# Kernel optimization log

Measured on AMD Instinct MI355X. Metric: run time of the kernel, lower is better.

The kernel has to match this reference:

```python
import jax, jax.numpy as jnp
import numpy as np
import math

B, L, WIN, D, H, FF, NL, V, M = 16, 2048, 128, 512, 8, 2048, 3, 32000, 32
HD = D // H
EPS = 1e-5
RECON_W = 0.1

def _ln(x, g, b):
    m = x.mean(-1, keepdims=True)
    v = ((x - m) ** 2).mean(-1, keepdims=True)
    return (x - m) * jax.lax.rsqrt(v + EPS) * g + b

def _denoiser(x_t, t, motif, left, right, glob, time_proj_W, time_proj_b, cond_proj_W, cond_proj_b,
              qkv_W, qkv_b, attn_out_W, attn_out_b, ff1_W, ff1_b, ff2_W, ff2_b,
              ln1_g, ln1_b, ln2_g, ln2_b, out_W, out_b):
    half = D // 2
    freqs = jnp.exp(-math.log(10000.0) * jnp.arange(half) / (half - 1))
    a = t[:, None] * freqs[None, :]
    temb = jnp.concatenate([jnp.sin(a), jnp.cos(a)], -1) @ time_proj_W.T + time_proj_b
    x = x_t + temb[:, None, :]
    cond = jnp.concatenate([motif, left, right, glob], -1) @ cond_proj_W.T + cond_proj_b
    x = jnp.concatenate([cond[:, None, :], x], 1)
    S = x.shape[1]
    for i in range(NL):  # post-norm TransformerEncoderLayer, relu, no dropout (eval)
        qkv = x @ qkv_W[i].T + qkv_b[i]
        q, k, v = jnp.split(qkv, 3, axis=-1)
        q = q.reshape(B, S, H, HD); k = k.reshape(B, S, H, HD); v = v.reshape(B, S, H, HD)
        attn = jax.nn.softmax(jnp.einsum('bqhd,bkhd->bhqk', q, k) / math.sqrt(HD), axis=-1)
        ctx = jnp.einsum('bhqk,bkhd->bqhd', attn, v).reshape(B, S, D)
        x = _ln(x + ctx @ attn_out_W[i].T + attn_out_b[i], ln1_g[i], ln1_b[i])
        h = jax.nn.relu(x @ ff1_W[i].T + ff1_b[i]) @ ff2_W[i].T + ff2_b[i]
        x = _ln(x + h, ln2_g[i], ln2_b[i])
    return x[:, 1:, :] @ out_W.T + out_b

def setup_inputs():
    key = jax.random.key(0)
    ks = jax.random.split(key, 20)
    s = 0.02
    inp = {}
    inp['token_ids'] = jax.random.randint(ks[0], (B, L), 0, V)
    inp['motif_ids'] = jax.random.randint(ks[1], (B, M), 0, V)
    inp['motif_len'] = jax.random.randint(ks[2], (B,), 1, M + 1)
    inp['window_start'] = jax.random.randint(ks[3], (B,), 0, L - WIN)
    lens = jax.random.randint(ks[4], (B,), 1, WIN + 1).at[0].set(WIN)
    inp['window_end'] = inp['window_start'] + lens
    inp['t'] = jax.random.uniform(ks[5], (B,))
    inp['x0'] = jax.random.normal(ks[6], (B, WIN, D))
    inp['embed_table'] = jax.random.normal(ks[7], (V, D)) * s
    inp['decode_W'] = jax.random.normal(ks[8], (V, D)) * s
    inp['decode_b'] = jnp.zeros((V,))
    inp['adapter_W'] = jax.random.normal(ks[9], (D, D)) * s
    inp['adapter_b'] = jnp.zeros((D,))
    inp['time_proj_W'] = jax.random.normal(ks[10], (D, D)) * s
    inp['time_proj_b'] = jnp.zeros((D,))
    inp['cond_proj_W'] = jax.random.normal(ks[11], (D, 4 * D)) * s
    inp['cond_proj_b'] = jnp.zeros((D,))
    inp['qkv_W'] = jax.random.normal(ks[12], (NL, 3 * D, D)) * s
    inp['qkv_b'] = jnp.zeros((NL, 3 * D))
    inp['attn_out_W'] = jax.random.normal(ks[13], (NL, D, D)) * s
    inp['attn_out_b'] = jnp.zeros((NL, D))
    inp['ff1_W'] = jax.random.normal(ks[14], (NL, FF, D)) * s
    inp['ff1_b'] = jnp.zeros((NL, FF))
    inp['ff2_W'] = jax.random.normal(ks[15], (NL, D, FF)) * s
    inp['ff2_b'] = jnp.zeros((NL, D))
    inp['ln1_g'] = jnp.ones((NL, D)); inp['ln1_b'] = jnp.zeros((NL, D))
    inp['ln2_g'] = jnp.ones((NL, D)); inp['ln2_b'] = jnp.zeros((NL, D))
    inp['out_W'] = jax.random.normal(ks[16], (D, D)) * s
    inp['out_b'] = jnp.zeros((D,))
    return inp

def _forward(token_ids, motif_ids, motif_len, window_start, window_end, t, x0,
             embed_table, decode_W, decode_b, adapter_W, adapter_b, den):
    hidden = embed_table[token_ids]  # frozen backbone encode: [B, L, D]
    pos = jnp.arange(L)
    def pool(s, e):  # vectorized masked mean over region [s, e)
        m = ((pos[None, :] >= s[:, None]) & (pos[None, :] < e[:, None])).astype(hidden.dtype)
        return jnp.einsum('bl,bld->bd', m, hidden) / jnp.maximum(m.sum(1, keepdims=True), 1.0)
    left = pool(jnp.zeros_like(window_start), window_start)
    right = pool(window_end, jnp.full_like(window_end, L))
    glob = hidden.mean(1)
    memb = embed_table[motif_ids]
    mmask = (jnp.arange(M)[None, :] < motif_len[:, None]).astype(memb.dtype)
    motif = (memb * mmask[..., None]).sum(1) / jnp.maximum(motif_len.astype(memb.dtype), 1.0)[:, None]
    actual = jnp.clip(window_end - window_start, 0, WIN)
    win_mask = jnp.arange(WIN)[None, :] < actual[:, None]
    idx = jnp.clip(window_start[:, None] + jnp.arange(WIN)[None, :], 0, L - 1)
    x1 = jnp.take_along_axis(hidden, idx[:, :, None], axis=1) * win_mask[..., None]
    x_t = (1 - t[:, None, None]) * x0 + t[:, None, None] * x1
    target_v = x1 - x0
    pred_v = _denoiser(x_t, t, motif, left, right, glob, *den)
    valid = win_mask[..., None].astype(x1.dtype)
    vel = (((pred_v - target_v) ** 2) * valid).sum() / (jnp.maximum(valid.sum(), 1.0) * D)
    pred_x1 = x_t + (1 - t[:, None, None]) * pred_v
    logits = (pred_x1 @ adapter_W.T + adapter_b) @ decode_W.T + decode_b
    labels = jnp.where(win_mask, jnp.take_along_axis(token_ids, idx, axis=1), -100)
    lv = labels != -100
    logp = jax.nn.log_softmax(logits, axis=-1)
    picked = jnp.take_along_axis(logp, jnp.maximum(labels, 0)[..., None], axis=-1)[..., 0]
    recon = -(picked * lv).sum() / jnp.maximum(lv.sum(), 1)
    return vel + RECON_W * recon

def reference(token_ids, motif_ids, motif_len, window_start, window_end, t, x0,
              embed_table, decode_W, decode_b, adapter_W, adapter_b,
              time_proj_W, time_proj_b, cond_proj_W, cond_proj_b, qkv_W, qkv_b,
              attn_out_W, attn_out_b, ff1_W, ff1_b, ff2_W, ff2_b,
              ln1_g, ln1_b, ln2_g, ln2_b, out_W, out_b):
    den = (time_proj_W, time_proj_b, cond_proj_W, cond_proj_b, qkv_W, qkv_b,
           attn_out_W, attn_out_b, ff1_W, ff1_b, ff2_W, ff2_b,
           ln1_g, ln1_b, ln2_g, ln2_b, out_W, out_b)
    return _forward(token_ids, motif_ids, motif_len, window_start, window_end, t, x0,
                    embed_table, decode_W, decode_b, adapter_W, adapter_b, den)
```

## Files before the change

kernel.cpp:

```cpp
#include <hip/hip_runtime.h>
#include <hip/hip_bf16.h>
#include <math.h>

typedef __hip_bfloat16 bf16;

constexpr int cB = 16, cL = 2048, cWIN = 128, cD = 512, cH = 8, cFF = 2048;
constexpr int cNL = 3, cV = 32000, cM = 32;
constexpr int cHD = cD / cH;
constexpr int cS = cWIN + 1;
constexpr float cEPS = 1e-5f;
constexpr float cRECON_W = 0.1f;
constexpr int cNVT = cV / 128;

__device__ __forceinline__ float b2f(bf16 x) { return __bfloat162float(x); }

__device__ __forceinline__ float ldx(const void* p, size_t i, int f32) {
    return f32 ? ((const float*)p)[i]
               : __bfloat162float(((const bf16*)p)[i]);
}

__device__ __forceinline__ unsigned int f2bf(float f) {
    union { float f; unsigned int u; } v; v.f = f;
    unsigned int u = v.u + 0x7FFFu + ((v.u >> 16) & 1u);
    return u >> 16;
}

__device__ __forceinline__ void glds16(const unsigned short* g, unsigned short* l) {
    __builtin_amdgcn_global_load_lds(
        (const __attribute__((address_space(1))) void*)g,
        (__attribute__((address_space(3))) void*)l, 16, 0, 0);
}

typedef short bf16x8 __attribute__((ext_vector_type(8)));
typedef float f32x4  __attribute__((ext_vector_type(4)));

__global__ void detect_kernel(const void* __restrict__ x0raw, int* __restrict__ flag)
{
    const unsigned short* h = (const unsigned short*)x0raw;
    int tid = threadIdx.x;
    int cnt = 0;
    for (int j = tid; j < 8192; j += 256) {
        unsigned short u = h[2 * j];
        int e = (u >> 7) & 0xFF;
        if (e >= 134) cnt++;
    }
    __shared__ int red[256];
    red[tid] = cnt; __syncthreads();
    for (int off = 128; off > 0; off >>= 1) {
        if (tid < off) red[tid] += red[tid + off];
        __syncthreads();
    }
    if (tid == 0) *flag = (red[0] > 400) ? 1 : 0;
}

__global__ __launch_bounds__(512) void pools_part_kernel(
    const int* __restrict__ tok, const int* __restrict__ wstart,
    const int* __restrict__ wend, const void* __restrict__ emb,
    float* __restrict__ part, const int* __restrict__ dflag)
{
    const int f32 = *dflag;
    int chunk = blockIdx.x;
    int b = blockIdx.y;
    int d = threadIdx.x;
    int ws_ = wstart[b], we_ = wend[b];
    float sl = 0.f, sr = 0.f, sg = 0.f;
    int l0 = chunk * 256;
    for (int l = l0; l < l0 + 256; ++l) {
        int t = tok[b * cL + l];
        float h = ldx(emb, (size_t)t * cD + d, f32);
        sg += h;
        if (l < ws_) sl += h;
        if (l >= we_) sr += h;
    }
    size_t base = ((size_t)(b * 8 + chunk)) * 3 * cD;
    part[base + d]            = sl;
    part[base + cD + d]       = sr;
    part[base + 2 * cD + d]   = sg;
}

__global__ __launch_bounds__(512) void pools_combine_kernel(
    const float* __restrict__ part, const int* __restrict__ mids,
    const int* __restrict__ mlen, const int* __restrict__ wstart,
    const int* __restrict__ wend, const void* __restrict__ emb,
    unsigned short* __restrict__ featb, const int* __restrict__ dflag)
{
    const int f32 = *dflag;
    int b = blockIdx.x;
    int d = threadIdx.x;
    int ws_ = wstart[b], we_ = wend[b];
    float sl = 0.f, sr = 0.f, sg = 0.f;
    for (int c = 0; c < 8; ++c) {
        size_t base = ((size_t)(b * 8 + c)) * 3 * cD;
        sl += part[base + d];
        sr += part[base + cD + d];
        sg += part[base + 2 * cD + d];
    }
    int ml = mlen[b];
    float sm = 0.f;
    for (int j = 0; j < cM; ++j) {
        if (j < ml) sm += ldx(emb, (size_t)mids[b * cM + j] * cD + d, f32);
    }
    unsigned short* fr = featb + (size_t)b * (4 * cD);
    fr[d]            = (unsigned short)f2bf(sm / fmaxf((float)ml, 1.f));
    fr[cD + d]       = (unsigned short)f2bf(sl / fmaxf((float)ws_, 1.f));
    fr[2 * cD + d]   = (unsigned short)f2bf(sr / fmaxf((float)(cL - we_), 1.f));
    fr[3 * cD + d]   = (unsigned short)f2bf(sg / (float)cL);
}

__global__ __launch_bounds__(512) void tf_kernel(
    const void* __restrict__ t_arr, unsigned short* __restrict__ tfbb,
    const int* __restrict__ dflag)
{
    const int f32 = *dflag;
    int b = blockIdx.x;
    int j = threadIdx.x;
    float t = ldx(t_arr, b, f32);
    const int half = cD / 2;
    float v;
    if (j < half) {
        float fr = expf(-logf(10000.f) * (float)j / (float)(half - 1));
        v = sinf(t * fr);
    } else {
        float fr = expf(-logf(10000.f) * (float)(j - half) / (float)(half - 1));
        v = cosf(t * fr);
    }
    tfbb[(size_t)b * cD + j] = (unsigned short)f2bf(v);
}

__global__ __launch_bounds__(512) void build_x_kernel(
    const int* __restrict__ tok, const int* __restrict__ wstart,
    const int* __restrict__ wend, const void* __restrict__ t_arr,
    const void* __restrict__ x0, const void* __restrict__ emb,
    const float* __restrict__ cond, const float* __restrict__ temb,
    float* __restrict__ x, unsigned short* __restrict__ xbf,
    float* __restrict__ x1, float* __restrict__ xt,
    const int* __restrict__ dflag)
{
    const int f32 = *dflag;
    int row = blockIdx.x;
    int b = row / cS, s = row % cS;
    int d = threadIdx.x;
    if (s == 0) {
        float cv = cond[b * cD + d];
        x[(size_t)row * cD + d] = cv;
        xbf[(size_t)row * cD + d] = (unsigned short)f2bf(cv);
        return;
    }
    int i = s - 1;
    int ws_ = wstart[b], we_ = wend[b];
    int actual = min(max(we_ - ws_, 0), cWIN);
    int idx = min(ws_ + i, cL - 1);
    float x1v = 0.f;
    if (i < actual) x1v = ldx(emb, (size_t)tok[b * cL + idx] * cD + d, f32);
    float t = ldx(t_arr, b, f32);
    float x0v = ldx(x0, ((size_t)b * cWIN + i) * cD + d, f32);
    float xtv = (1.f - t) * x0v + t * x1v;
    size_t ro = ((size_t)b * cWIN + i) * cD + d;
    x1[ro] = x1v;
    xt[ro] = xtv;
    float xv = xtv + temb[b * cD + d];
    x[(size_t)row * cD + d] = xv;
    xbf[(size_t)row * cD + d] = (unsigned short)f2bf(xv);
}

constexpr int GL2 = 72;
__global__ __launch_bounds__(256) void gemm_bf(
    const unsigned short* __restrict__ Abf, const void* __restrict__ Wb,
    size_t wOff, const void* __restrict__ biasb, size_t bOff,
    float* __restrict__ Cf, unsigned short* __restrict__ Cbf,
    int Mdim, int Ndim, int Kdim, int relu, int obf, int amap,
    const int* __restrict__ dflag)
{
    const int f32 = *dflag;
    const float* Wf = (const float*)Wb + wOff;
    const unsigned short* Wh = (const unsigned short*)Wb + wOff;
    __shared__ unsigned short As[2][64 * GL2];
    __shared__ unsigned short Bs[2][64 * GL2];
    const int tid = threadIdx.x;
    const int lane = tid & 63;
    const int wid = tid >> 6;
    const int wm = wid >> 1, wn = wid & 1;
    const int quad = lane >> 4, lm = lane & 15;
    const int m0 = blockIdx.y * 64;
    const int n0 = blockIdx.x * 64;

    f32x4 acc[2][2];
    #pragma unroll
    for (int i = 0; i < 2; ++i)
        #pragma unroll
        for (int j = 0; j < 2; ++j)
            acc[i][j] = (f32x4){0.f, 0.f, 0.f, 0.f};

    uint4 ra[2], rb[2];
    const int srow = tid >> 3;
    const int sc8  = (tid & 7) * 8;
    const int ssw  = ((tid & 7) ^ ((tid >> 3) & 7)) * 8;
    const int lmm  = lm & 7;

    auto loadA = [&](int k0) {
        #pragma unroll
        for (int t = 0; t < 2; ++t) {
            int r0 = m0 + srow + t * 32;
            uint4 v = {0u, 0u, 0u, 0u};
            if (r0 < Mdim) {
                size_t ar = amap ? ((size_t)(r0 >> 7) * cS + 1 + (r0 & 127))
                                 : (size_t)r0;
                v = *(const uint4*)(Abf + ar * Kdim + k0 + sc8);
            }
            ra[t] = v;
        }
    };
    auto loadB = [&](int k0) {
        #pragma unroll
        for (int t = 0; t < 2; ++t) {
            int row = srow + t * 32;
            size_t g = (size_t)(n0 + row) * Kdim + k0 + sc8;
            if (f32) {
                float4 v0 = *(const float4*)(Wf + g);
                float4 v1 = *(const float4*)(Wf + g + 4);
                rb[t] = make_uint4(
                    f2bf(v0.x) | (f2bf(v0.y) << 16), f2bf(v0.z) | (f2bf(v0.w) << 16),
                    f2bf(v1.x) | (f2bf(v1.y) << 16), f2bf(v1.z) | (f2bf(v1.w) << 16));
            } else {
                rb[t] = *(const uint4*)(Wh + g);
            }
        }
    };

    loadA(0); loadB(0);
    const int nk = Kdim >> 6;
    for (int t = 0; t < nk; ++t) {
        const int buf = t & 1;
        #pragma unroll
        for (int u = 0; u < 2; ++u) {
            *(uint4*)(&As[buf][(srow + u * 32) * GL2 + ssw]) = ra[u];
            *(uint4*)(&Bs[buf][(srow + u * 32) * GL2 + ssw]) = rb[u];
        }
        __syncthreads();
        if (t + 1 < nk) { loadA((t + 1) * 64); loadB((t + 1) * 64); }
        #pragma unroll
        for (int kk = 0; kk < 2; ++kk) {
            const int sl = ((kk * 4 + quad) ^ lmm) * 8;
            bf16x8 a0 = *(const bf16x8*)(&As[buf][(wm * 32 + lm) * GL2 + sl]);
            bf16x8 a1 = *(const bf16x8*)(&As[buf][(wm * 32 + 16 + lm) * GL2 + sl]);
            bf16x8 b0 = *(const bf16x8*)(&Bs[buf][(wn * 32 + lm) * GL2 + sl]);
            bf16x8 b1 = *(const bf16x8*)(&Bs[buf][(wn * 32 + 16 + lm) * GL2 + sl]);
            acc[0][0] = __builtin_amdgcn_mfma_f32_16x16x32_bf16(a0, b0, acc[0][0], 0, 0, 0);
            acc[0][1] = __builtin_amdgcn_mfma_f32_16x16x32_bf16(a0, b1, acc[0][1], 0, 0, 0);
            acc[1][0] = __builtin_amdgcn_mfma_f32_16x16x32_bf16(a1, b0, acc[1][0], 0, 0, 0);
            acc[1][1] = __builtin_amdgcn_mfma_f32_16x16x32_bf16(a1, b1, acc[1][1], 0, 0, 0);
        }
    }

    #pragma unroll
    for (int in = 0; in < 2; ++in) {
        int gc = n0 + wn * 32 + in * 16 + lm;
        float bv = ldx(biasb, bOff + gc, f32);
        #pragma unroll
        for (int im = 0; im < 2; ++im) {
            #pragma unroll
            for (int r = 0; r < 4; ++r) {
                int gr = m0 + wm * 32 + im * 16 + quad * 4 + r;
                if (gr < Mdim) {
                    float v = acc[im][in][r] + bv;
                    if (relu) v = fmaxf(v, 0.f);
                    if (obf) Cbf[(size_t)gr * Ndim + gc] = (unsigned short)f2bf(v);
                    else     Cf[(size_t)gr * Ndim + gc] = v;
                }
            }
        }
    }
}

__global__ __launch_bounds__(256) void attn_mfma_kernel(
    const unsigned short* __restrict__ qkv, unsigned short* __restrict__ ctx)
{
    constexpr int SP = 160;
    constexpr int KP = 72;
    constexpr int VP = 168;
    const int h = blockIdx.x, b = blockIdx.y;
    const int tid = threadIdx.x;
    const int lane = tid & 63;
    const int wid = tid >> 6;
    const int quad = lane >> 4, lm = lane & 15;

    __shared__ unsigned short Ks[SP * KP];
    __shared__ unsigned short Vt[64 * VP];
    __shared__ unsigned short Pl[4 * 16 * VP];

    const unsigned short* base = qkv + (size_t)b * cS * (3 * cD) + h * cHD;

    for (int c = tid; c < SP * 8; c += 256) {
        int row = c >> 3, g = c & 7;
        uint4 v = {0u, 0u, 0u, 0u};
        if (row < cS)
            v = *(const uint4*)(base + (size_t)row * (3 * cD) + cD + g * 8);
        *(uint4*)(Ks + row * KP + g * 8) = v;
    }
    for (int c = tid; c < SP * 16; c += 256) {
        int key = c >> 4, d4 = c & 15;
        uint2 v = {0u, 0u};
        if (key < cS)
            v = *(const uint2*)(base + (size_t)key * (3 * cD) + 2 * cD + d4 * 4);
        Vt[(d4 * 4 + 0) * VP + key] = (unsigned short)(v.x & 0xFFFFu);
        Vt[(d4 * 4 + 1) * VP + key] = (unsigned short)(v.x >> 16);
        Vt[(d4 * 4 + 2) * VP + key] = (unsigned short)(v.y & 0xFFFFu);
        Vt[(d4 * 4 + 3) * VP + key] = (unsigned short)(v.y >> 16);
    }
    __syncthreads();

    unsigned short* Pw = Pl + wid * (16 * VP);

    for (int t = wid; t < 9; t += 4) {
        int qs = t * 16 + lm;
        bf16x8 aq[2];
        #pragma unroll
        for (int j = 0; j < 8; ++j) { aq[0][j] = 0; aq[1][j] = 0; }
        if (qs < cS) {
            const unsigned short* qrow = base + (size_t)qs * (3 * cD);
            aq[0] = *(const bf16x8*)(qrow + quad * 8);
            aq[1] = *(const bf16x8*)(qrow + 32 + quad * 8);
        }

        f32x4 sc[10];
        #pragma unroll
        for (int n = 0; n < 10; ++n) {
            sc[n] = (f32x4){0.f, 0.f, 0.f, 0.f};
            bf16x8 bk0 = *(const bf16x8*)(Ks + (n * 16 + lm) * KP + quad * 8);
            sc[n] = __builtin_amdgcn_mfma_f32_16x16x32_bf16(aq[0], bk0, sc[n], 0, 0, 0);
            bf16x8 bk1 = *(const bf16x8*)(Ks + (n * 16 + lm) * KP + 32 + quad * 8);
            sc[n] = __builtin_amdgcn_mfma_f32_16x16x32_bf16(aq[1], bk1, sc[n], 0, 0, 0);
        }

        #pragma unroll
        for (int r = 0; r < 4; ++r) {
            float mx = -3.0e38f;
            #pragma unroll
            for (int n = 0; n < 10; ++n) {
                float v = sc[n][r] * 0.125f;
                mx = fmaxf(mx, ((n * 16 + lm) < cS) ? v : -3.0e38f);
            }
            #pragma unroll
            for (int msk = 1; msk < 16; msk <<= 1)
                mx = fmaxf(mx, __shfl_xor(mx, msk));
            float p[10];
            float sum = 0.f;
            #pragma unroll
            for (int n = 0; n < 10; ++n) {
                float e = ((n * 16 + lm) < cS) ? expf(sc[n][r] * 0.125f - mx) : 0.f;
                p[n] = e; sum += e;
            }
            #pragma unroll
            for (int msk = 1; msk < 16; msk <<= 1)
                sum += __shfl_xor(sum, msk);
            float inv = 1.f / sum;
            unsigned short* pr = Pw + (quad * 4 + r) * VP + lm;
            #pragma unroll
            for (int n = 0; n < 10; ++n)
                pr[n * 16] = (unsigned short)f2bf(p[n] * inv);
        }

        asm volatile("s_waitcnt lgkmcnt(0)" ::: "memory");
        __builtin_amdgcn_sched_barrier(0);

        f32x4 o[4];
        #pragma unroll
        for (int j = 0; j < 4; ++j) o[j] = (f32x4){0.f, 0.f, 0.f, 0.f};
        #pragma unroll
        for (int ks = 0; ks < 5; ++ks) {
            bf16x8 ap = *(const bf16x8*)(Pw + lm * VP + ks * 32 + quad * 8);
            #pragma unroll
            for (int j = 0; j < 4; ++j) {
                bf16x8 bv = *(const bf16x8*)(Vt + (j * 16 + lm) * VP + ks * 32 + quad * 8);
                o[j] = __builtin_amdgcn_mfma_f32_16x16x32_bf16(ap, bv, o[j], 0, 0, 0);
            }
        }

        #pragma unroll
        for (int r = 0; r < 4; ++r) {
            int s_ = t * 16 + quad * 4 + r;
            if (s_ < cS) {
                unsigned short* orow = ctx + ((size_t)(b * cS + s_)) * cD + h * cHD;
                #pragma unroll
                for (int j = 0; j < 4; ++j)
                    orow[j * 16 + lm] = (unsigned short)f2bf(o[j][r]);
            }
        }
    }
}

__global__ __launch_bounds__(256) void resid_ln_kernel(
    float* __restrict__ x, const float* __restrict__ h,
    const void* __restrict__ g, const void* __restrict__ bta, size_t off,
    unsigned short* __restrict__ xbf, const int* __restrict__ dflag)
{
    const int f32 = *dflag;
    int row = blockIdx.x;
    int tid = threadIdx.x;
    __shared__ float red[256];
    float v[2];
    float s = 0.f;
    #pragma unroll
    for (int j = 0; j < 2; ++j) {
        int d = tid + j * 256;
        v[j] = x[(size_t)row * cD + d] + h[(size_t)row * cD + d];
        s += v[j];
    }
    red[tid] = s; __syncthreads();
    for (int o = 128; o > 0; o >>= 1) {
        if (tid < o) red[tid] += red[tid + o];
        __syncthreads();
    }
    float mean = red[0] / (float)cD;
    __syncthreads();
    float vs = 0.f;
    #pragma unroll
    for (int j = 0; j < 2; ++j) { float dd = v[j] - mean; vs += dd * dd; }
    red[tid] = vs; __syncthreads();
    for (int o = 128; o > 0; o >>= 1) {
        if (tid < o) red[tid] += red[tid + o];
        __syncthreads();
    }
    float rs = rsqrtf(red[0] / (float)cD + cEPS);
    #pragma unroll
    for (int j = 0; j < 2; ++j) {
        int d = tid + j * 256;
        float ov = (v[j] - mean) * rs * ldx(g, off + d, f32) + ldx(bta, off + d, f32);
        x[(size_t)row * cD + d] = ov;
        xbf[(size_t)row * cD + d] = (unsigned short)f2bf(ov);
    }
}

__global__ __launch_bounds__(512) void predvel_kernel(
    const float* __restrict__ xt, const float* __restrict__ pv,
    const float* __restrict__ x1, const void* __restrict__ x0,
    const void* __restrict__ t_arr, const int* __restrict__ wstart,
    const int* __restrict__ wend, unsigned short* __restrict__ px1,
    float* __restrict__ velpart, const int* __restrict__ dflag)
{
    const int f32 = *dflag;
    int row = blockIdx.x;
    int b = row >> 7, i = row & 127;
    int d = threadIdx.x;
    float t = ldx(t_arr, b, f32);
    size_t o = (size_t)row * cD + d;
    float pvv = pv[o];
    px1[o] = (unsigned short)f2bf(xt[o] + (1.f - t) * pvv);
    int actual = min(max(wend[b] - wstart[b], 0), cWIN);
    float s = 0.f;
    if (i < actual) {
        float tv = x1[o] - ldx(x0, o, f32);
        float diff = pvv - tv;
        s = diff * diff;
    }
    __shared__ float red[512];
    red[d] = s; __syncthreads();
    for (int off = 256; off > 0; off >>= 1) {
        if (d < off) red[d] += red[d + off];
        __syncthreads();
    }
    if (d == 0) velpart[row] = red[0];
}

__global__ void labels_kernel(
    const int* __restrict__ tok, const int* __restrict__ wstart,
    const int* __restrict__ wend, int* __restrict__ labels)
{
    int r = blockIdx.x * 256 + threadIdx.x;
    if (r >= cB * cWIN) return;
    int b = r / cWIN, i = r % cWIN;
    int ws_ = wstart[b], we_ = wend[b];
    int actual = min(max(we_ - ws_, 0), cWIN);
    labels[r] = (i < actual) ? tok[b * cL + min(ws_ + i, cL - 1)] : -1;
}

__global__ __launch_bounds__(256) void cvt_w_kernel(
    const void* __restrict__ Wsrc, unsigned short* __restrict__ dst,
    const int* __restrict__ dflag)
{
    if (!*dflag) return;
    const float4* src = (const float4*)Wsrc;
    size_t n4 = (size_t)cV * cD / 4;
    for (size_t i = (size_t)blockIdx.x * 256 + threadIdx.x; i < n4;
         i += (size_t)gridDim.x * 256) {
        float4 v = src[i];
        unsigned int p0 = f2bf(v.x) | (f2bf(v.y) << 16);
        unsigned int p1 = f2bf(v.z) | (f2bf(v.w) << 16);
        ((uint2*)dst)[i] = make_uint2(p0, p1);
    }
}

__global__ __launch_bounds__(256) void decode_mfma2_kernel(
    const unsigned short* __restrict__ hbf, const unsigned short* __restrict__ wbf,
    const void* __restrict__ dW, const void* __restrict__ db,
    const int* __restrict__ labels,
    float* __restrict__ pm, float* __restrict__ ps, float* __restrict__ lab,
    const int* __restrict__ dflag)
{
    const int f32 = *dflag;
    const unsigned short* Wsrc = f32 ? wbf : (const unsigned short*)dW;
    const int bid = blockIdx.x;
    const int xcd = bid & 7;
    const int local = bid >> 3;
    const int nt = xcd * 32 + (local >> 4);
    const int mt = local & 15;
    if (nt >= cNVT) return;
    const int m0 = mt * 128, n0 = nt * 128;

    __shared__ __align__(16) char smem[17408];
    unsigned short* As = (unsigned short*)smem;
    unsigned short* Bs = As + 4096;

    const int tid = threadIdx.x;
    const int lane = tid & 63;
    const int wid = tid >> 6;
    const int wm = wid >> 1, wn = wid & 1;
    const int quad = lane >> 4, lm = lane & 15;

    const int grow  = lane >> 2;
    const int gslot = (lane & 3) ^ ((lane >> 3) & 3);
    const int rslot = (quad ^ ((lm >> 1) & 3)) * 8;

    const unsigned short* gA = hbf  + (size_t)(m0 + wid * 32 + grow) * cD + gslot * 8;
    const unsigned short* gB = Wsrc + (size_t)(n0 + wid * 32 + grow) * cD + gslot * 8;

    f32x4 acc[4][4];
    #pragma unroll
    for (int i = 0; i < 4; ++i)
        #pragma unroll
        for (int j = 0; j < 4; ++j)
            acc[i][j] = (f32x4){0.f, 0.f, 0.f, 0.f};

    for (int k0 = 0; k0 < cD; k0 += 32) {
        #pragma unroll
        for (int c = 0; c < 2; ++c) {
            glds16(gA + (size_t)c * 16 * cD + k0, As + (wid * 2 + c) * 512);
            glds16(gB + (size_t)c * 16 * cD + k0, Bs + (wid * 2 + c) * 512);
        }
        __syncthreads();
        bf16x8 af[4], bfr[4];
        #pragma unroll
        for (int im = 0; im < 4; ++im)
            af[im] = *(const bf16x8*)(As + (wm * 64 + im * 16 + lm) * 32 + rslot);
        #pragma unroll
        for (int in = 0; in < 4; ++in)
            bfr[in] = *(const bf16x8*)(Bs + (wn * 64 + in * 16 + lm) * 32 + rslot);
        #pragma unroll
        for (int im = 0; im < 4; ++im)
            #pragma unroll
            for (int in = 0; in < 4; ++in)
                acc[im][in] = __builtin_amdgcn_mfma_f32_16x16x32_bf16(
                    af[im], bfr[in], acc[im][in], 0, 0, 0);
        __syncthreads();
    }

    float bv[4];
    #pragma unroll
    for (int in = 0; in < 4; ++in)
        bv[in] = ldx(db, n0 + wn * 64 + in * 16 + lm, f32);
    #pragma unroll
    for (int im = 0; im < 4; ++im)
        #pragma unroll
        for (int in = 0; in < 4; ++in)
            #pragma unroll
            for (int r = 0; r < 4; ++r)
                acc[im][in][r] += bv[in];

    #pragma unroll
    for (int im = 0; im < 4; ++im) {
        #pragma unroll
        for (int r = 0; r < 4; ++r) {
            int gr = m0 + wm * 64 + im * 16 + quad * 4 + r;
            int lb = labels[gr];
            #pragma unroll
            for (int in = 0; in < 4; ++in) {
                int col = n0 + wn * 64 + in * 16 + lm;
                if (lb == col) lab[gr] = acc[im][in][r];
            }
        }
    }

    float (*red)[33] = (float(*)[33])smem;
    float* mrow = (float*)(smem + 16896);
    #pragma unroll
    for (int im = 0; im < 4; ++im) {
        #pragma unroll
        for (int r = 0; r < 4; ++r) {
            int rl = wm * 64 + im * 16 + quad * 4 + r;
            float mx = acc[im][0][r];
            #pragma unroll
            for (int in = 1; in < 4; ++in) mx = fmaxf(mx, acc[im][in][r]);
            red[rl][wn * 16 + lm] = mx;
        }
    }
    __syncthreads();
    if (tid < 128) {
        float mx = red[tid][0];
        #pragma unroll
        for (int t = 1; t < 32; ++t) mx = fmaxf(mx, red[tid][t]);
        mrow[tid] = mx;
    }
    __syncthreads();
    #pragma unroll
    for (int im = 0; im < 4; ++im) {
        #pragma unroll
        for (int r = 0; r < 4; ++r) {
            int rl = wm * 64 + im * 16 + quad * 4 + r;
            float m_ = mrow[rl];
            float s = 0.f;
            #pragma unroll
            for (int in = 0; in < 4; ++in) s += expf(acc[im][in][r] - m_);
            red[rl][wn * 16 + lm] = s;
        }
    }
    __syncthreads();
    if (tid < 128) {
        float s = red[tid][0];
        #pragma unroll
        for (int t = 1; t < 32; ++t) s += red[tid][t];
        int gr = m0 + tid;
        pm[(size_t)gr * cNVT + nt] = mrow[tid];
        ps[(size_t)gr * cNVT + nt] = s;
    }
}

constexpr int GLDS = 40;
__global__ __launch_bounds__(256) void decode_mfma_kernel(
    const unsigned short* __restrict__ hbf, const void* __restrict__ dW,
    const void* __restrict__ db, const int* __restrict__ labels,
    float* __restrict__ pm, float* __restrict__ ps, float* __restrict__ lab,
    const int* __restrict__ dflag)
{
    const int f32 = *dflag;
    const float* Wf = (const float*)dW;
    const unsigned short* Wh = (const unsigned short*)dW;
    __shared__ unsigned short As[128 * GLDS];
    __shared__ unsigned short Bs[128 * GLDS];
    const int tid = threadIdx.x;
    const int lane = tid & 63;
    const int wid = tid >> 6;
    const int wm = wid >> 1, wn = wid & 1;
    const int quad = lane >> 4, lm = lane & 15;
    const int nt = blockIdx.x;
    const int mt = blockIdx.y;
    const int m0 = mt * 128, n0 = nt * 128;

    f32x4 acc[4][4];
    #pragma unroll
    for (int i = 0; i < 4; ++i)
        #pragma unroll
        for (int j = 0; j < 4; ++j)
            acc[i][j] = (f32x4){0.f, 0.f, 0.f, 0.f};

    for (int k0 = 0; k0 < cD; k0 += 32) {
        #pragma unroll
        for (int t = 0; t < 2; ++t) {
            int idx = tid + t * 256;
            int row = idx >> 2, c = idx & 3;
            uint4 v = *(const uint4*)(hbf + (size_t)(m0 + row) * cD + k0 + c * 8);
            *(uint4*)(As + row * GLDS + c * 8) = v;
        }
        #pragma unroll
        for (int t = 0; t < 4; ++t) {
            int chunk = tid + t * 256;
            int row = chunk >> 3;
            int kc = (chunk & 7) * 4;
            size_t gro = (size_t)(n0 + row) * cD + k0 + kc;
            if (f32) {
                float4 v = *(const float4*)(Wf + gro);
                unsigned int p0 = f2bf(v.x) | (f2bf(v.y) << 16);
                unsigned int p1 = f2bf(v.z) | (f2bf(v.w) << 16);
                *(uint2*)(Bs + row * GLDS + kc) = make_uint2(p0, p1);
            } else {
                *(uint2*)(Bs + row * GLDS + kc) = *(const uint2*)(Wh + gro);
            }
        }
        __syncthreads();
        bf16x8 af[4], bfr[4];
        #pragma unroll
        for (int im = 0; im < 4; ++im) {
            int row = wm * 64 + im * 16 + lm;
            af[im] = *(const bf16x8*)(As + row * GLDS + quad * 8);
        }
        #pragma unroll
        for (int in = 0; in < 4; ++in) {
            int row = wn * 64 + in * 16 + lm;
            bfr[in] = *(const bf16x8*)(Bs + row * GLDS + quad * 8);
        }
        #pragma unroll
        for (int im = 0; im < 4; ++im)
            #pragma unroll
            for (int in = 0; in < 4; ++in)
                acc[im][in] = __builtin_amdgcn_mfma_f32_16x16x32_bf16(
                    af[im], bfr[in], acc[im][in], 0, 0, 0);
        __syncthreads();
    }

    float bv[4];
    #pragma unroll
    for (int in = 0; in < 4; ++in)
        bv[in] = ldx(db, n0 + wn * 64 + in * 16 + lm, f32);
    #pragma unroll
    for (int im = 0; im < 4; ++im)
        #pragma unroll
        for (int in = 0; in < 4; ++in)
            #pragma unroll
            for (int r = 0; r < 4; ++r)
                acc[im][in][r] += bv[in];

    #pragma unroll
    for (int im = 0; im < 4; ++im) {
        #pragma unroll
        for (int r = 0; r < 4; ++r) {
            int gr = m0 + wm * 64 + im * 16 + quad * 4 + r;
            int lb = labels[gr];
            #pragma unroll
            for (int in = 0; in < 4; ++in) {
                int col = n0 + wn * 64 + in * 16 + lm;
                if (lb == col) lab[gr] = acc[im][in][r];
            }
        }
    }

    __shared__ float red[128][33];
    __shared__ float mrow[128];
    #pragma unroll
    for (int im = 0; im < 4; ++im) {
        #pragma unroll
        for (int r = 0; r < 4; ++r) {
            int rl = wm * 64 + im * 16 + quad * 4 + r;
            float mx = acc[im][0][r];
            #pragma unroll
            for (int in = 1; in < 4; ++in) mx = fmaxf(mx, acc[im][in][r]);
            red[rl][wn * 16 + lm] = mx;
        }
    }
    __syncthreads();
    if (tid < 128) {
        float mx = red[tid][0];
        #pragma unroll
        for (int t = 1; t < 32; ++t) mx = fmaxf(mx, red[tid][t]);
        mrow[tid] = mx;
    }
    __syncthreads();
    #pragma unroll
    for (int im = 0; im < 4; ++im) {
        #pragma unroll
        for (int r = 0; r < 4; ++r) {
            int rl = wm * 64 + im * 16 + quad * 4 + r;
            float m_ = mrow[rl];
            float s = 0.f;
            #pragma unroll
            for (int in = 0; in < 4; ++in) s += expf(acc[im][in][r] - m_);
            red[rl][wn * 16 + lm] = s;
        }
    }
    __syncthreads();
    if (tid < 128) {
        float s = red[tid][0];
        #pragma unroll
        for (int t = 1; t < 32; ++t) s += red[tid][t];
        int gr = m0 + tid;
        pm[(size_t)gr * cNVT + nt] = mrow[tid];
        ps[(size_t)gr * cNVT + nt] = s;
    }
}

__global__ __launch_bounds__(64) void lse_reduce_kernel(
    const float* __restrict__ pm, const float* __restrict__ ps,
    const float* __restrict__ lab, const int* __restrict__ labels,
    float* __restrict__ logppart)
{
    int r = blockIdx.x;
    int tid = threadIdx.x;
    if (labels[r] < 0) {
        if (tid == 0) logppart[r] = 0.f;
        return;
    }
    float m = -1e30f;
    for (int c = tid; c < cNVT; c += 64) m = fmaxf(m, pm[(size_t)r * cNVT + c]);
    for (int off = 32; off > 0; off >>= 1) m = fmaxf(m, __shfl_down(m, off));
    m = __shfl(m, 0);
    float s = 0.f;
    for (int c = tid; c < cNVT; c += 64)
        s += ps[(size_t)r * cNVT + c] * expf(pm[(size_t)r * cNVT + c] - m);
    for (int off = 32; off > 0; off >>= 1) s += __shfl_down(s, off);
    if (tid == 0) logppart[r] = lab[r] - (m + logf(s));
}

__global__ __launch_bounds__(256) void finalize_kernel(
    const float* __restrict__ velpart, const float* __restrict__ logppart,
    const int* __restrict__ wstart, const int* __restrict__ wend,
    void* __restrict__ out, const int* __restrict__ dflag)
{
    const int f32 = *dflag;
    __shared__ float r1[256], r2[256];
    int tid = threadIdx.x;
    float s1 = 0.f, s2 = 0.f;
    for (int r = tid; r < cB * cWIN; r += 256) {
        s1 += velpart[r];
        s2 += logppart[r];
    }
    r1[tid] = s1; r2[tid] = s2; __syncthreads();
    for (int off = 128; off > 0; off >>= 1) {
        if (tid < off) { r1[tid] += r1[tid + off]; r2[tid] += r2[tid + off]; }
        __syncthreads();
    }
    if (tid == 0) {
        float cnt = 0.f;
        for (int b = 0; b < cB; ++b)
            cnt += (float)min(max(wend[b] - wstart[b], 0), cWIN);
        cnt = fmaxf(cnt, 1.f);
        float vel = r1[0] / (cnt * (float)cD);
        float recon = -r2[0] / cnt;
        float loss = vel + cRECON_W * recon;
        if (f32) ((float*)out)[0] = loss;
        else     ((bf16*)out)[0] = __float2bfloat16(loss);
    }
}

extern "C" void kernel_launch(void* const* d_in, const int* in_sizes, int n_in,
                              void* d_out, int out_size, void* d_ws, size_t ws_size,
                              hipStream_t stream) {
    const int*  token_ids    = (const int*)d_in[0];
    const int*  motif_ids    = (const int*)d_in[1];
    const int*  motif_len    = (const int*)d_in[2];
    const int*  window_start = (const int*)d_in[3];
    const int*  window_end   = (const int*)d_in[4];
    const void* t_arr        = d_in[5];
    const void* x0           = d_in[6];
    const void* embed_table  = d_in[7];
    const void* decode_W     = d_in[8];
    const void* decode_b     = d_in[9];
    const void* adapter_W    = d_in[10];
    const void* adapter_b    = d_in[11];
    const void* time_proj_W  = d_in[12];
    const void* time_proj_b  = d_in[13];
    const void* cond_proj_W  = d_in[14];
    const void* cond_proj_b  = d_in[15];
    const void* qkv_W        = d_in[16];
    const void* qkv_b        = d_in[17];
    const void* attn_out_W   = d_in[18];
    const void* attn_out_b   = d_in[19];
    const void* ff1_W        = d_in[20];
    const void* ff1_b        = d_in[21];
    const void* ff2_W        = d_in[22];
    const void* ff2_b        = d_in[23];
    const void* ln1_g        = d_in[24];
    const void* ln1_b        = d_in[25];
    const void* ln2_g        = d_in[26];
    const void* ln2_b        = d_in[27];
    const void* out_W        = d_in[28];
    const void* out_b        = d_in[29];

    float* w = (float*)d_ws;
    const size_t SZ_X   = (size_t)cB * cS * cD;
    const size_t SZ_BA  = (size_t)cB * cS * cFF;
    const size_t SZ_ROW = (size_t)cB * cWIN * cD;
    float* x     = w;
    float* bufA  = x + SZ_X;
    float* bufB  = bufA + SZ_BA;
    float* bufC  = bufB + SZ_X;
    float* x1b   = bufC + SZ_X;
    float* xtb   = x1b + SZ_ROW;
    float* pvb   = xtb + SZ_ROW;
    float* h2b   = pvb + SZ_ROW;
    float* feat  = h2b + SZ_ROW;
    float* tfb   = feat + (size_t)cB * 4 * cD;
    float* cond  = tfb + (size_t)cB * cD;
    float* temb  = cond + (size_t)cB * cD;
    float* velpart = temb + (size_t)cB * cD;
    float* logppart = velpart + (size_t)cB * cWIN;
    int*   dflag = (int*)(logppart + (size_t)cB * cWIN);
    float* wsend = (float*)(dflag + 16);
    unsigned short* wbf = (unsigned short*)wsend;

    const size_t need_bytes = ((char*)wsend - (char*)d_ws)
                            + (size_t)cV * cD * sizeof(unsigned short) + 256;
    const bool fast_decode = ws_size >= need_bytes;

    const int Wrows = cB * cWIN;
    const int Mrows = cB * cS;

    unsigned short* xbf    = (unsigned short*)h2b;
    unsigned short* featbf = xbf + (size_t)Mrows * cD;
    unsigned short* tfbbf  = featbf + (size_t)cB * 4 * cD;
    unsigned short* qkvbf  = (unsigned short*)bufA;
    unsigned short* ff1bf  = (unsigned short*)bufA;
    unsigned short* ctxbf  = (unsigned short*)bufB;
    unsigned short* px1bf  = (unsigned short*)(bufA + (size_t)3 * 1024 * 1024);
    unsigned short* hbf    = (unsigned short*)bufC;

    float* pm  = bufA;
    float* ps  = pm + (size_t)Wrows * cNVT;
    float* lab = ps + (size_t)Wrows * cNVT;
    int*   labels = (int*)(lab + Wrows);
    float* poolspart = bufC;

    auto gemm = [&](const unsigned short* A, const void* W, size_t wOff,
                    const void* bias, size_t bOff, float* Cf, unsigned short* Cbf,
                    int M_, int N_, int K_, int relu, int obf, int amap) {
        dim3 grid(N_ / 64, (M_ + 63) / 64);
        gemm_bf<<<grid, 256, 0, stream>>>(A, W, wOff, bias, bOff, Cf, Cbf,
                                          M_, N_, K_, relu, obf, amap, dflag);
    };

    detect_kernel<<<1, 256, 0, stream>>>(x0, dflag);
    if (fast_decode)
        cvt_w_kernel<<<4096, 256, 0, stream>>>(decode_W, wbf, dflag);
    pools_part_kernel<<<dim3(8, cB), cD, 0, stream>>>(token_ids, window_start,
        window_end, embed_table, poolspart, dflag);
    pools_combine_kernel<<<cB, cD, 0, stream>>>(poolspart, motif_ids, motif_len,
        window_start, window_end, embed_table, featbf, dflag);
    tf_kernel<<<cB, cD, 0, stream>>>(t_arr, tfbbf, dflag);
    gemm(featbf, cond_proj_W, 0, cond_proj_b, 0, cond, nullptr, cB, cD, 4 * cD, 0, 0, 0);
    gemm(tfbbf, time_proj_W, 0, time_proj_b, 0, temb, nullptr, cB, cD, cD, 0, 0, 0);
    build_x_kernel<<<Mrows, cD, 0, stream>>>(token_ids, window_start, window_end,
        t_arr, x0, embed_table, cond, temb, x, xbf, x1b, xtb, dflag);

    for (int i = 0; i < cNL; ++i) {
        gemm(xbf, qkv_W, (size_t)i * 3 * cD * cD, qkv_b, (size_t)i * 3 * cD,
             nullptr, qkvbf, Mrows, 3 * cD, cD, 0, 1, 0);
        attn_mfma_kernel<<<dim3(cH, cB), 256, 0, stream>>>(qkvbf, ctxbf);
        gemm(ctxbf, attn_out_W, (size_t)i * cD * cD, attn_out_b, (size_t)i * cD,
             bufC, nullptr, Mrows, cD, cD, 0, 0, 0);
        resid_ln_kernel<<<Mrows, 256, 0, stream>>>(x, bufC, ln1_g, ln1_b,
             (size_t)i * cD, xbf, dflag);
        gemm(xbf, ff1_W, (size_t)i * cFF * cD, ff1_b, (size_t)i * cFF,
             nullptr, ff1bf, Mrows, cFF, cD, 1, 1, 0);
        gemm(ff1bf, ff2_W, (size_t)i * cD * cFF, ff2_b, (size_t)i * cD,
             bufC, nullptr, Mrows, cD, cFF, 0, 0, 0);
        resid_ln_kernel<<<Mrows, 256, 0, stream>>>(x, bufC, ln2_g, ln2_b,
             (size_t)i * cD, xbf, dflag);
    }

    gemm(xbf, out_W, 0, out_b, 0, pvb, nullptr, Wrows, cD, cD, 0, 0, 1);
    predvel_kernel<<<Wrows, 512, 0, stream>>>(xtb, pvb, x1b, x0, t_arr,
        window_start, window_end, px1bf, velpart, dflag);
    gemm(px1bf, adapter_W, 0, adapter_b, 0, nullptr, hbf, Wrows, cD, cD, 0, 1, 0);

    labels_kernel<<<(Wrows + 255) / 256, 256, 0, stream>>>(
        token_ids, window_start, window_end, labels);
    if (fast_decode) {
        decode_mfma2_kernel<<<4096, 256, 0, stream>>>(
            hbf, wbf, decode_W, decode_b, labels, pm, ps, lab, dflag);
    } else {
        decode_mfma_kernel<<<dim3(cNVT, Wrows / 128), 256, 0, stream>>>(
            hbf, decode_W, decode_b, labels, pm, ps, lab, dflag);
    }
    lse_reduce_kernel<<<Wrows, 64, 0, stream>>>(pm, ps, lab, labels, logppart);

    finalize_kernel<<<1, 256, 0, stream>>>(velpart, logppart,
        window_start, window_end, d_out, dflag);
}
```

Measured before the change: 964.5 us.

## Retune pools split, GEMM prefetch, attention grid split, and decode GEMM K-tile

Several independent changes land together. The pooling reduction is split into 16 chunks instead of 8, and the generic GEMM now uses two register sets so global loads run two K-steps ahead. The attention kernel gets a third grid dimension so each block handles only 3 query tiles, which raises parallelism but reloads K/V per block and leaves one wave idle. The decode GEMM uses a 64-wide K tile with a new swizzle, halving barriers but doubling LDS, and the weight-conversion grid is halved.

```diff
diff --git a/kernel.cpp b/kernel.cpp
--- a/kernel.cpp
+++ b/kernel.cpp
@@ -64,15 +64,15 @@
     int d = threadIdx.x;
     int ws_ = wstart[b], we_ = wend[b];
     float sl = 0.f, sr = 0.f, sg = 0.f;
-    int l0 = chunk * 256;
-    for (int l = l0; l < l0 + 256; ++l) {
+    int l0 = chunk * 128;
+    for (int l = l0; l < l0 + 128; ++l) {
         int t = tok[b * cL + l];
         float h = ldx(emb, (size_t)t * cD + d, f32);
         sg += h;
         if (l < ws_) sl += h;
         if (l >= we_) sr += h;
     }
-    size_t base = ((size_t)(b * 8 + chunk)) * 3 * cD;
+    size_t base = ((size_t)(b * 16 + chunk)) * 3 * cD;
     part[base + d]            = sl;
     part[base + cD + d]       = sr;
     part[base + 2 * cD + d]   = sg;
@@ -89,8 +89,8 @@
     int d = threadIdx.x;
     int ws_ = wstart[b], we_ = wend[b];
     float sl = 0.f, sr = 0.f, sg = 0.f;
-    for (int c = 0; c < 8; ++c) {
-        size_t base = ((size_t)(b * 8 + c)) * 3 * cD;
+    for (int c = 0; c < 16; ++c) {
+        size_t base = ((size_t)(b * 16 + c)) * 3 * cD;
         sl += part[base + d];
         sr += part[base + cD + d];
         sg += part[base + 2 * cD + d];
@@ -191,13 +191,12 @@
         for (int j = 0; j < 2; ++j)
             acc[i][j] = (f32x4){0.f, 0.f, 0.f, 0.f};
 
-    uint4 ra[2], rb[2];
     const int srow = tid >> 3;
     const int sc8  = (tid & 7) * 8;
     const int ssw  = ((tid & 7) ^ ((tid >> 3) & 7)) * 8;
     const int lmm  = lm & 7;
 
-    auto loadA = [&](int k0) {
+    auto loadA = [&](int k0, uint4* r) {
         #pragma unroll
         for (int t = 0; t < 2; ++t) {
             int r0 = m0 + srow + t * 32;
@@ -207,10 +206,10 @@
                                  : (size_t)r0;
                 v = *(const uint4*)(Abf + ar * Kdim + k0 + sc8);
             }
-            ra[t] = v;
+            r[t] = v;
         }
     };
-    auto loadB = [&](int k0) {
+    auto loadB = [&](int k0, uint4* r) {
         #pragma unroll
         for (int t = 0; t < 2; ++t) {
             int row = srow + t * 32;
@@ -218,26 +217,22 @@
             if (f32) {
                 float4 v0 = *(const float4*)(Wf + g);
                 float4 v1 = *(const float4*)(Wf + g + 4);
-                rb[t] = make_uint4(
+                r[t] = make_uint4(
                     f2bf(v0.x) | (f2bf(v0.y) << 16), f2bf(v0.z) | (f2bf(v0.w) << 16),
                     f2bf(v1.x) | (f2bf(v1.y) << 16), f2bf(v1.z) | (f2bf(v1.w) << 16));
             } else {
-                rb[t] = *(const uint4*)(Wh + g);
+                r[t] = *(const uint4*)(Wh + g);
             }
         }
     };
-
-    loadA(0); loadB(0);
-    const int nk = Kdim >> 6;
-    for (int t = 0; t < nk; ++t) {
-        const int buf = t & 1;
+    auto stores = [&](int buf, const uint4* ra, const uint4* rb) {
         #pragma unroll
         for (int u = 0; u < 2; ++u) {
             *(uint4*)(&As[buf][(srow + u * 32) * GL2 + ssw]) = ra[u];
             *(uint4*)(&Bs[buf][(srow + u * 32) * GL2 + ssw]) = rb[u];
         }
-        __syncthreads();
-        if (t + 1 < nk) { loadA((t + 1) * 64); loadB((t + 1) * 64); }
+    };
+    auto compute = [&](int buf) {
         #pragma unroll
         for (int kk = 0; kk < 2; ++kk) {
             const int sl = ((kk * 4 + quad) ^ lmm) * 8;
@@ -250,6 +245,21 @@
             acc[1][0] = __builtin_amdgcn_mfma_f32_16x16x32_bf16(a1, b0, acc[1][0], 0, 0, 0);
             acc[1][1] = __builtin_amdgcn_mfma_f32_16x16x32_bf16(a1, b1, acc[1][1], 0, 0, 0);
         }
+    };
+
+    uint4 raA[2], rbA[2], raB[2], rbB[2];
+    loadA(0, raA);  loadB(0, rbA);
+    loadA(64, raB); loadB(64, rbB);
+    const int nk = Kdim >> 6;
+    for (int t = 0; t < nk; t += 2) {
+        stores(0, raA, rbA);
+        __syncthreads();
+        if (t + 2 < nk) { loadA((t + 2) * 64, raA); loadB((t + 2) * 64, rbA); }
+        compute(0);
+        stores(1, raB, rbB);
+        __syncthreads();
+        if (t + 3 < nk) { loadA((t + 3) * 64, raB); loadB((t + 3) * 64, rbB); }
+        compute(1);
     }
 
     #pragma unroll
@@ -278,7 +288,7 @@
     constexpr int SP = 160;
     constexpr int KP = 72;
     constexpr int VP = 168;
-    const int h = blockIdx.x, b = blockIdx.y;
+    const int h = blockIdx.x, b = blockIdx.y, z = blockIdx.z;
     const int tid = threadIdx.x;
     const int lane = tid & 63;
     const int wid = tid >> 6;
@@ -310,8 +320,9 @@
     __syncthreads();
 
     unsigned short* Pw = Pl + wid * (16 * VP);
-
-    for (int t = wid; t < 9; t += 4) {
+    const int t = z * 3 + wid;
+
+    if (wid < 3 && t < 9) {
         int qs = t * 16 + lm;
         bf16x8 aq[2];
         #pragma unroll
@@ -507,9 +518,9 @@
     if (nt >= cNVT) return;
     const int m0 = mt * 128, n0 = nt * 128;
 
-    __shared__ __align__(16) char smem[17408];
+    __shared__ __align__(16) char smem[32768];
     unsigned short* As = (unsigned short*)smem;
-    unsigned short* Bs = As + 4096;
+    unsigned short* Bs = As + 8192;
 
     const int tid = threadIdx.x;
     const int lane = tid & 63;
@@ -517,9 +528,9 @@
     const int wm = wid >> 1, wn = wid & 1;
     const int quad = lane >> 4, lm = lane & 15;
 
-    const int grow  = lane >> 2;
-    const int gslot = (lane & 3) ^ ((lane >> 3) & 3);
-    const int rslot = (quad ^ ((lm >> 1) & 3)) * 8;
+    const int grow  = lane >> 3;
+    const int gslot = (lane & 7) ^ grow;
+    const int lmm   = lm & 7;
 
     const unsigned short* gA = hbf  + (size_t)(m0 + wid * 32 + grow) * cD + gslot * 8;
     const unsigned short* gB = Wsrc + (size_t)(n0 + wid * 32 + grow) * cD + gslot * 8;
@@ -531,26 +542,30 @@
         for (int j = 0; j < 4; ++j)
             acc[i][j] = (f32x4){0.f, 0.f, 0.f, 0.f};
 
-    for (int k0 = 0; k0 < cD; k0 += 32) {
-        #pragma unroll
-        for (int c = 0; c < 2; ++c) {
-            glds16(gA + (size_t)c * 16 * cD + k0, As + (wid * 2 + c) * 512);
-            glds16(gB + (size_t)c * 16 * cD + k0, Bs + (wid * 2 + c) * 512);
-        }
-        __syncthreads();
-        bf16x8 af[4], bfr[4];
-        #pragma unroll
-        for (int im = 0; im < 4; ++im)
-            af[im] = *(const bf16x8*)(As + (wm * 64 + im * 16 + lm) * 32 + rslot);
-        #pragma unroll
-        for (int in = 0; in < 4; ++in)
-            bfr[in] = *(const bf16x8*)(Bs + (wn * 64 + in * 16 + lm) * 32 + rslot);
-        #pragma unroll
-        for (int im = 0; im < 4; ++im)
+    for (int k0 = 0; k0 < cD; k0 += 64) {
+        #pragma unroll
+        for (int c = 0; c < 4; ++c) {
+            glds16(gA + (size_t)c * 8 * cD + k0, As + (wid * 4 + c) * 512);
+            glds16(gB + (size_t)c * 8 * cD + k0, Bs + (wid * 4 + c) * 512);
+        }
+        __syncthreads();
+        #pragma unroll
+        for (int kk = 0; kk < 2; ++kk) {
+            const int sl = ((kk * 4 + quad) ^ lmm) * 8;
+            bf16x8 af[4], bfr[4];
+            #pragma unroll
+            for (int im = 0; im < 4; ++im)
+                af[im] = *(const bf16x8*)(As + (wm * 64 + im * 16 + lm) * 64 + sl);
             #pragma unroll
             for (int in = 0; in < 4; ++in)
-                acc[im][in] = __builtin_amdgcn_mfma_f32_16x16x32_bf16(
-                    af[im], bfr[in], acc[im][in], 0, 0, 0);
+                bfr[in] = *(const bf16x8*)(Bs + (wn * 64 + in * 16 + lm) * 64 + sl);
+            #pragma unroll
+            for (int im = 0; im < 4; ++im)
+                #pragma unroll
+                for (int in = 0; in < 4; ++in)
+                    acc[im][in] = __builtin_amdgcn_mfma_f32_16x16x32_bf16(
+                        af[im], bfr[in], acc[im][in], 0, 0, 0);
+        }
         __syncthreads();
     }
 
@@ -907,8 +922,8 @@
 
     detect_kernel<<<1, 256, 0, stream>>>(x0, dflag);
     if (fast_decode)
-        cvt_w_kernel<<<4096, 256, 0, stream>>>(decode_W, wbf, dflag);
-    pools_part_kernel<<<dim3(8, cB), cD, 0, stream>>>(token_ids, window_start,
+        cvt_w_kernel<<<2048, 256, 0, stream>>>(decode_W, wbf, dflag);
+    pools_part_kernel<<<dim3(16, cB), cD, 0, stream>>>(token_ids, window_start,
         window_end, embed_table, poolspart, dflag);
     pools_combine_kernel<<<cB, cD, 0, stream>>>(poolspart, motif_ids, motif_len,
         window_start, window_end, embed_table, featbf, dflag);
@@ -921,7 +936,7 @@
     for (int i = 0; i < cNL; ++i) {
         gemm(xbf, qkv_W, (size_t)i * 3 * cD * cD, qkv_b, (size_t)i * 3 * cD,
              nullptr, qkvbf, Mrows, 3 * cD, cD, 0, 1, 0);
-        attn_mfma_kernel<<<dim3(cH, cB), 256, 0, stream>>>(qkvbf, ctxbf);
+        attn_mfma_kernel<<<dim3(cH, cB, 3), 256, 0, stream>>>(qkvbf, ctxbf);
         gemm(ctxbf, attn_out_W, (size_t)i * cD * cD, attn_out_b, (size_t)i * cD,
              bufC, nullptr, Mrows, cD, cD, 0, 0, 0);
         resid_ln_kernel<<<Mrows, 256, 0, stream>>>(x, bufC, ln1_g, ln1_b,
```

Measured after the change: 933.5 us. -3.2%, faster.
